# Performance work log

Hardware: AMD Instinct MI355X
Metric: run time of the kernel (lower is better)

Reference implementation:

```python
import jax, jax.numpy as jnp
import numpy as np


def _fwd_diffs(x, D, scale):
    # forward difference along each of the first D axes, zero at the end, scaled by x.shape[0]
    outs = []
    for d in range(D):
        pad = [(0, 0)] * x.ndim
        pad[d] = (0, 1)
        outs.append(jnp.pad(jnp.diff(x, axis=d), pad) * scale)
    return jnp.stack(outs, 0)


def _bwd_diffs(p, scale):
    # p: [D, *dims, l]; backward difference of p[i] along axis i with the torch narrow/cat semantics
    outs = []
    for i in range(p.shape[0]):
        pi = p[i]
        head = jax.lax.slice_in_dim(pi, 0, pi.shape[i] - 1, axis=i)
        z = jnp.zeros_like(jax.lax.slice_in_dim(pi, 0, 1, axis=i))
        before = jnp.concatenate([head, z], axis=i)
        after = jnp.concatenate([z, head], axis=i)
        outs.append((before - after) * scale)
    return jnp.stack(outs, 0)


def _solver(f, repeats, l, lmbda, nu):
    dims = list(f.shape)
    H = dims[0]
    D = len(dims) - 1
    res = 1.0 / H
    tauu = res / 6.0
    sigmap = res / (3.0 + l)
    sigmas = 1.0
    proj = l * (l - 1) // 2 + l
    tau = 1.0 / (2.0 + proj / 4.0)
    # (k1,k2) interval combinations and the membership matrix M[K,z] = (k1<=z<=k2)
    combos = np.array([(a, b) for a in range(l) for b in range(a, l)], dtype=np.int32)
    k1 = jnp.asarray(combos[:, 0])
    k2 = jnp.asarray(combos[:, 1])
    zz = np.arange(l)
    M = jnp.asarray(((combos[:, :1] <= zz) & (zz <= combos[:, 1:2])).astype(np.float32))  # [proj, l]

    img = jnp.broadcast_to(f[..., None], tuple(dims) + (l,))
    klf = jnp.arange(1, l + 1, dtype=f.dtype) / l - img  # k/l - f
    u = img
    ubar = img
    px = jnp.zeros((D,) + tuple(dims) + (l,), f.dtype)
    pt = jnp.zeros(tuple(dims) + (l,), f.dtype)
    sx = jnp.zeros((D,) + tuple(dims) + (proj,), f.dtype)
    mux = sx
    mubarx = sx
    nrj = jnp.zeros((), f.dtype)
    h_un = u

    for it in range(int(repeats)):
        # ---- parabola: dual ascent on (px,pt) with closed-form cubic (Cardano) projection ----
        musum = jnp.einsum('...p,pz->...z', mux, M)
        ux = px + sigmap * (_fwd_diffs(ubar, D, H) + musum)
        ut = pt + sigmap * (jnp.pad(jnp.diff(ubar, axis=-1), [(0, 0)] * (ubar.ndim - 1) + [(0, 1)]) * l)
        pen = lmbda * klf * klf
        B = 0.25 * jnp.sum(ux * ux, axis=0) - pen
        mask = ut < B
        y = ut + pen
        norm = jnp.sqrt(jnp.sum(ux * ux, axis=0))
        a = 0.5 * norm                                   # 2*0.25*norm
        b = (2.0 / 3.0) * (1.0 - 0.5 * y)
        sb = jnp.sqrt(jnp.maximum(-b, 0.0))              # sqrt(-b), only used where b<0
        d = jnp.where(b < 0, (a - sb ** 3) * (a + sb ** 3), a * a + b ** 3)
        c = jnp.power(a + jnp.sqrt(jnp.maximum(d, 0.0)), 1.0 / 3.0)
        mask1 = (d >= 0) & (c == 0)
        mask3 = d < 0
        sb3 = jnp.where(sb > 0, sb ** 3, 1.0)
        ratio = jnp.clip(a / sb3, -1.0, 1.0)
        c_safe = jnp.where(c == 0, 1.0, c)
        v = jnp.where(mask1, 0.0,
                      jnp.where(mask3, 2.0 * sb * jnp.cos(jnp.arccos(ratio) / 3.0), c - b / c_safe))
        norm_safe = jnp.where(norm == 0, 1.0, norm)
        px = jnp.where(mask[None],
                       jnp.where((norm == 0)[None], 0.0, (2.0 * v / norm_safe)[None] * ux),
                       ux)
        pt = jnp.where(mask, 0.25 * jnp.sum(px * px, axis=0) - pen, ut)

        # ---- l2 projection of s ----
        mx = sx - sigmas * mubarx
        snorm = jnp.sqrt(jnp.sum(mx * mx, axis=0))
        snorm_safe = jnp.where(snorm == 0, 1.0, snorm)
        sx = jnp.where((snorm > nu * H)[None], mx * nu / snorm_safe[None], mx)

        # ---- mu update: per-(k1,k2) partial sums over the label axis via cumsum ----
        cs = jnp.cumsum(px, axis=-1)
        cs = jnp.pad(cs, [(0, 0)] * (px.ndim - 1) + [(1, 0)])
        t = cs[..., k2 + 1] - cs[..., k1]                # [D, *dims, proj]
        mux_new = mux + tau * (sx - t)
        mubarx = 2.0 * mux_new - mux
        mux = mux_new

        # ---- clipping: primal update with box projection and boundary conditions ----
        if it % 10 == 0:
            h_un = u
        dx = _bwd_diffs(px, H)
        head = pt[..., :-1]
        z = jnp.zeros_like(pt[..., :1])
        dt = (jnp.concatenate([head, z], axis=-1) - jnp.concatenate([z, head], axis=-1)) * l
        Dv = u + tauu * (jnp.sum(dx, axis=0) + dt)
        un = jnp.clip(Dv, 0.0, 1.0)
        un = un.at[..., 0].set(1.0).at[..., l - 1].set(0.0)
        ubar = 2.0 * un - u
        u = un
        if it % 10 == 0:
            nrj = jnp.sum(jnp.abs(u - h_un))
    return u, nrj


def setup_inputs() -> dict:
    key = jax.random.key(0)
    H, W = 256, 256
    f = jax.random.uniform(key, (H, W, 1), dtype=jnp.float32)
    return {"f": f, "repeats": 10, "l": 16, "lmbda": 0.5, "nu": 0.1, "tol": 0.0}


def reference(f, repeats, l, lmbda, nu, tol):
    # tol/early-exit: tol=0 so the torch break never fires; iteration count is fixed at `repeats`.
    u, nrj = _solver(f, repeats, l, lmbda, nu)
    denom = float(np.prod(f.shape[:-1])) * l
    return (u, nrj, nrj / denom, 0)
```

## Files before the change

### kernel.cpp

```cpp
#include <hip/hip_runtime.h>

#define HH 256
#define WW 256
#define NPIX (HH*WW)
#define LL 16
#define NL (NPIX*LL)
#define PP 136
#define PP2 (PP*2)

typedef _Float16 half_t;
typedef __attribute__((ext_vector_type(8))) _Float16 half8;

static constexpr float SIGMAP_F = (float)((1.0/256.0)/(3.0+16.0));
static constexpr float TAUU_F   = (float)((1.0/256.0)/6.0);
static constexpr float TAU_F    = (float)(1.0/36.0);

__device__ __forceinline__ float clampf(float x, float lo, float hi){
    return fminf(fmaxf(x, lo), hi);
}
__device__ __forceinline__ half8 h8zero() {
    half8 v;
    #pragma unroll
    for (int i = 0; i < 8; ++i) v[i] = (half_t)0.0f;
    return v;
}

template<int MODE>
__global__ __launch_bounds__(256) void k_prox(const float* __restrict__ f,
    const half_t* __restrict__ ubar,
    const half_t* __restrict__ pxOld,
    half_t* __restrict__ pxCur,
    half_t* __restrict__ pt,
    const half_t* __restrict__ musum,
    float* __restrict__ nrj)
{
    int t = blockIdx.x*256 + threadIdx.x;
    if (MODE == 0 && t == 0) *nrj = 0.0f;
    int n  = t >> 1;
    int hf = t & 1;
    int z0 = hf << 3;
    int i = n >> 8, j = n & (WW-1);
    bool iok = (i < HH-1), jok = (j < WW-1);
    size_t base = (size_t)n*LL + z0;

    float fv = f[n];
    float g0c = 0.0f, g1c = 0.0f;
    half8 ubv = h8zero(), ubi = h8zero(), ubj = h8zero();
    float ubz8 = 0.0f;
    half8 ms0v = h8zero(), ms1v = h8zero();
    half8 p0v  = h8zero(), p1v  = h8zero(), ptv = h8zero();
    if (MODE == 0) {
        g0c = iok ? (f[n + WW] - fv) * 256.0f : 0.0f;
        g1c = jok ? (f[n + 1]  - fv) * 256.0f : 0.0f;
    } else {
        ubv = *reinterpret_cast<const half8*>(ubar + base);
        if (iok) ubi = *reinterpret_cast<const half8*>(ubar + base + (size_t)WW*LL);
        if (jok) ubj = *reinterpret_cast<const half8*>(ubar + base + LL);
        if (hf == 0) ubz8 = (float)ubar[base + 8];
        ms0v = *reinterpret_cast<const half8*>(musum + base);
        ms1v = *reinterpret_cast<const half8*>(musum + NL + base);
        p0v  = *reinterpret_cast<const half8*>(pxOld + base);
        p1v  = *reinterpret_cast<const half8*>(pxOld + NL + base);
        ptv  = *reinterpret_cast<const half8*>(pt + base);
    }

    half8 o0, o1, opt;
    #pragma unroll
    for (int e = 0; e < 8; ++e) {
        int z = z0 + e;
        float ux0, ux1, ut;
        if (MODE == 0) {
            ux0 = SIGMAP_F * g0c;
            ux1 = SIGMAP_F * g1c;
            ut  = 0.0f;
        } else {
            float ub = (float)ubv[e];
            float g0 = iok ? ((float)ubi[e] - ub) * 256.0f : 0.0f;
            float g1 = jok ? ((float)ubj[e] - ub) * 256.0f : 0.0f;
            float ubn = (e < 7) ? (float)ubv[e+1] : ubz8;
            float gt = (z < LL-1) ? (ubn - ub) * 16.0f : 0.0f;
            ux0 = (float)p0v[e] + SIGMAP_F * (g0 + (float)ms0v[e]);
            ux1 = (float)p1v[e] + SIGMAP_F * (g1 + (float)ms1v[e]);
            ut  = (float)ptv[e] + SIGMAP_F * gt;
        }

        float klf = (float)(z + 1) * 0.0625f - fv;
        float pen = 0.5f * klf * klf;

        float n2 = ux0*ux0 + ux1*ux1;
        float B  = 0.25f * n2 - pen;
        bool mask = ut < B;

        float px0 = ux0, px1 = ux1, ptn = ut;
        if (mask) {
            float y    = ut + pen;
            float norm = sqrtf(n2);
            float a    = 0.5f * norm;
            float b    = (2.0f/3.0f) * (1.0f - 0.5f*y);
            float v;
            if (b < 0.0f) {
                float sb  = sqrtf(-b);
                float sb3 = sb*sb*sb;
                float dd  = (a - sb3)*(a + sb3);
                if (dd < 0.0f) {
                    float ratio = clampf(a / sb3, -1.0f, 1.0f);
                    v = 2.0f * sb * cosf(acosf(ratio) * (1.0f/3.0f));
                } else {
                    float c = cbrtf(a + sqrtf(dd));
                    v = (c == 0.0f) ? 0.0f : (c - b/c);
                }
            } else {
                float dd = a*a + b*b*b;
                float c  = cbrtf(a + sqrtf(dd));
                v = (c == 0.0f) ? 0.0f : (c - b/c);
            }
            if (norm == 0.0f) { px0 = 0.0f; px1 = 0.0f; }
            else              { float s = 2.0f*v/norm; px0 = s*ux0; px1 = s*ux1; }
            ptn = 0.25f*(px0*px0 + px1*px1) - pen;
        }
        o0[e]  = (half_t)px0;
        o1[e]  = (half_t)px1;
        opt[e] = (half_t)ptn;
    }
    *reinterpret_cast<half8*>(pxCur + base)      = o0;
    *reinterpret_cast<half8*>(pxCur + NL + base) = o1;
    *reinterpret_cast<half8*>(pt + base)         = opt;
}

#define PH(k)  ((k) < 8 ? (float)ph0[(k)] : (float)ph1[(k)-8])
#define PPV(k) ((k) < 8 ? (float)pp0[(k)] : (float)pp1[(k)-8])

template<int H, int MODE>
__device__ __forceinline__ void do_set(int d, int n, int lane,
    half8 ph0, half8 ph1, half8 pp0, half8 pp1,
    const half_t* __restrict__ muC,
    half_t* __restrict__ muO,
    float* __restrict__ part)
{
    constexpr size_t setbase = (size_t)H * 17 * 2 * NPIX;
    const size_t vb   = setbase + (size_t)n*16 + (size_t)d*8;
    const size_t vb1  = vb + (size_t)16*NPIX;
    const size_t tail = setbase + (size_t)32*NPIX + (size_t)n*2 + (size_t)d;

    half8 mCv0 = h8zero(), mCv1 = h8zero(), mOv0 = h8zero(), mOv1 = h8zero();
    float mCT = 0.0f, mOT = 0.0f;
    if (MODE >= 1) {
        mCv0 = *reinterpret_cast<const half8*>(&muC[vb]);
        mCv1 = *reinterpret_cast<const half8*>(&muC[vb1]);
        mCT  = (float)muC[tail];
    }
    if (MODE == 2) {
        mOv0 = *reinterpret_cast<const half8*>(&muO[vb]);
        mOv1 = *reinterpret_cast<const half8*>(&muO[vb1]);
        mOT  = (float)muO[tail];
    }

    float tsA = 0.0f, tsB = 0.0f, tpA = 0.0f, tpB = 0.0f;
    #pragma unroll
    for (int k = H; k < 16; ++k) tsA += PH(k);
    #pragma unroll
    for (int k = 15-H; k < 16; ++k) tsB += PH(k);
    if (MODE >= 1) {
        #pragma unroll
        for (int k = H; k < 16; ++k) tpA += PPV(k);
        #pragma unroll
        for (int k = 15-H; k < 16; ++k) tpB += PPV(k);
    }

    half8 muo0, muo1;
    half_t muoT = (half_t)0.0f;
    float sA = 0.0f, sB = 0.0f;
    int q = 0;

    #pragma unroll
    for (int z = 15; z >= 0; --z) {
        float m = 0.0f;
        if (z >= H) {
            float mn;
            if (MODE == 0) {
                mn = -TAU_F * tsA;
            } else {
                float mC, mO;
                if (q < 8)       { mC=(float)mCv0[q];   mO=(float)mOv0[q]; }
                else if (q < 16) { mC=(float)mCv1[q-8]; mO=(float)mOv1[q-8]; }
                else             { mC=mCT;              mO=mOT; }
                float sxp = (mC - mO) * 36.0f + tpA;
                float mx  = sxp - (2.0f*mC - mO);
                float mo  = __shfl_xor(mx, 1);
                float snorm = sqrtf(mx*mx + mo*mo);
                if (snorm > 25.6f) mx *= 0.1f / snorm;
                mn = mC + TAU_F*(mx - tsA);
            }
            if (q < 8)       muo0[q]   = (half_t)mn;
            else if (q < 16) muo1[q-8] = (half_t)mn;
            else             muoT      = (half_t)mn;
            sA += mn;
            m  += sA;
            ++q;
        }
        if (z >= 15-H) {
            float mn;
            if (MODE == 0) {
                mn = -TAU_F * tsB;
            } else {
                float mC, mO;
                if (q < 8)       { mC=(float)mCv0[q];   mO=(float)mOv0[q]; }
                else if (q < 16) { mC=(float)mCv1[q-8]; mO=(float)mOv1[q-8]; }
                else             { mC=mCT;              mO=mOT; }
                float sxp = (mC - mO) * 36.0f + tpB;
                float mx  = sxp - (2.0f*mC - mO);
                float mo  = __shfl_xor(mx, 1);
                float snorm = sqrtf(mx*mx + mo*mo);
                if (snorm > 25.6f) mx *= 0.1f / snorm;
                mn = mC + TAU_F*(mx - tsB);
            }
            if (q < 8)       muo0[q]   = (half_t)mn;
            else if (q < 16) muo1[q-8] = (half_t)mn;
            else             muoT      = (half_t)mn;
            sB += mn;
            m  += sB;
            ++q;
        }
        if (z >= H+1) {
            tsA -= PH(z);
            if (MODE >= 1) tpA -= PPV(z);
        }
        if (z >= 15-H+1) {
            tsB -= PH(z);
            if (MODE >= 1) tpB -= PPV(z);
        }
        part[H*1024 + z*64 + lane] = m;
    }

    *reinterpret_cast<half8*>(&muO[vb])  = muo0;
    *reinterpret_cast<half8*>(&muO[vb1]) = muo1;
    muO[tail] = muoT;
}

template<int MODE>
__global__ __launch_bounds__(512, 4) void k_smu_u(
    const float* __restrict__ f,
    const half_t* __restrict__ pxCur,
    const half_t* __restrict__ pxOld,
    const half_t* __restrict__ pt,
    const half_t* __restrict__ muC,
    half_t* __restrict__ muO,
    half_t* __restrict__ musum,
    float* __restrict__ u, half_t* __restrict__ ubar,
    float* __restrict__ out,
    float* __restrict__ nrj, int last)
{
    __shared__ float part[8192];
    __shared__ float wsum[8];

    int tid  = threadIdx.x;
    int wv   = tid >> 6;
    int lane = tid & 63;
    int pix  = lane >> 1;
    int d    = lane & 1;
    int n    = blockIdx.x*32 + pix;

    const half8* pv = reinterpret_cast<const half8*>(pxCur + (size_t)d*NL + (size_t)n*LL);
    half8 ph0 = pv[0], ph1 = pv[1];
    half8 pp0 = h8zero(), pp1 = h8zero();
    if (MODE >= 1) {
        const half8* ppv = reinterpret_cast<const half8*>(pxOld + (size_t)d*NL + (size_t)n*LL);
        pp0 = ppv[0]; pp1 = ppv[1];
    }

    if      (wv == 0) do_set<0,MODE>(d,n,lane,ph0,ph1,pp0,pp1,muC,muO,part);
    else if (wv == 1) do_set<1,MODE>(d,n,lane,ph0,ph1,pp0,pp1,muC,muO,part);
    else if (wv == 2) do_set<2,MODE>(d,n,lane,ph0,ph1,pp0,pp1,muC,muO,part);
    else if (wv == 3) do_set<3,MODE>(d,n,lane,ph0,ph1,pp0,pp1,muC,muO,part);
    else if (wv == 4) do_set<4,MODE>(d,n,lane,ph0,ph1,pp0,pp1,muC,muO,part);
    else if (wv == 5) do_set<5,MODE>(d,n,lane,ph0,ph1,pp0,pp1,muC,muO,part);
    else if (wv == 6) do_set<6,MODE>(d,n,lane,ph0,ph1,pp0,pp1,muC,muO,part);
    else              do_set<7,MODE>(d,n,lane,ph0,ph1,pp0,pp1,muC,muO,part);

    __syncthreads();

    int t  = blockIdx.x*512 + tid;
    int z  = t & (LL-1);
    int n2 = t >> 4;
    int i2 = n2 >> 8;
    int j2 = n2 & (WW-1);
    float p0c = (float)pxCur[t];
    float p1c = (float)pxCur[NL + t];
    float p0u = (i2 > 0) ? (float)pxCur[t - WW*LL] : 0.0f;
    float p1l = (j2 > 0) ? (float)pxCur[NL + t - LL] : 0.0f;
    float ptc = (float)pt[t];
    float ptm = (z > 0) ? (float)pt[t - 1] : 0.0f;
    float uo  = (MODE == 0) ? f[n2] : u[t];

    #pragma unroll
    for (int r = 0; r < 2; ++r) {
        int z2    = (tid >> 6) + r*8;
        int inner = tid & 63;
        float s = 0.0f;
        #pragma unroll
        for (int hh = 0; hh < 8; ++hh) s += part[hh*1024 + z2*64 + inner];
        int d2 = inner & 1, pix2 = inner >> 1;
        musum[(size_t)d2*NL + ((size_t)blockIdx.x*32 + pix2)*LL + z2] = (half_t)s;
    }

    {
        float d0 = ((i2 < HH-1) ? p0c : 0.0f) - p0u;
        float d1 = ((j2 < WW-1) ? p1c : 0.0f) - p1l;
        float dt = ((z < LL-1) ? ptc : 0.0f) - ptm;

        float Dv = uo + TAUU_F * ((d0 + d1) * 256.0f + dt * 16.0f);
        float un = clampf(Dv, 0.0f, 1.0f);
        if (z == 0)     un = 1.0f;
        if (z == LL-1)  un = 0.0f;
        if (last) out[t] = un;
        else {
            u[t]    = un;
            ubar[t] = (half_t)(2.0f*un - uo);
        }

        if (MODE == 0) {
            float v = fabsf(un - uo);
            #pragma unroll
            for (int off = 32; off > 0; off >>= 1) v += __shfl_down(v, off);
            if ((tid & 63) == 0) wsum[wv] = v;
            __syncthreads();
            if (tid == 0) {
                float s = 0.0f;
                #pragma unroll
                for (int q = 0; q < 8; ++q) s += wsum[q];
                atomicAdd(nrj, s);
            }
        }
    }
}

__global__ void k_final(const float* __restrict__ nrj, float* __restrict__ out_tail)
{
    if (threadIdx.x == 0) {
        float e = *nrj;
        out_tail[0] = e;
        out_tail[1] = e * (1.0f/1048576.0f);
        out_tail[2] = 0.0f;
    }
}

extern "C" void kernel_launch(void* const* d_in, const int* in_sizes, int n_in,
                              void* d_out, int out_size, void* d_ws, size_t ws_size,
                              hipStream_t stream)
{
    const float* f = (const float*)d_in[0];
    float* out = (float*)d_out;

    char* w = (char*)d_ws;
    size_t off = 0;
    auto allocf = [&](size_t nfloats) {
        float* p = (float*)(w + off);
        off += nfloats * sizeof(float);
        return p;
    };
    auto alloch = [&](size_t nhalf) {
        half_t* p = (half_t*)(w + off);
        off += nhalf * sizeof(half_t);
        return p;
    };
    half_t* muA    = alloch((size_t)NPIX * PP2);
    half_t* muB    = alloch((size_t)NPIX * PP2);
    half_t* musum  = alloch(2*(size_t)NL);
    half_t* pxA    = alloch(2*(size_t)NL);
    half_t* pxB    = alloch(2*(size_t)NL);
    half_t* pt     = alloch((size_t)NL);
    half_t* ubar   = alloch((size_t)NL);
    float*  u      = allocf((size_t)NL);
    float*  nrj    = allocf(64);
    (void)ws_size; (void)in_sizes; (void)n_in; (void)out_size;

    half_t* pxC = pxA;
    half_t* pxO = pxB;
    half_t* mC  = muA;
    half_t* mO  = muB;
    for (int it = 0; it < 10; ++it) {
        int last = (it == 9) ? 1 : 0;
        if (it == 0) {
            k_prox<0><<<2*NPIX/256, 256, 0, stream>>>(f, ubar, pxO, pxC, pt, musum, nrj);
            k_smu_u<0><<<NPIX/32, 512, 0, stream>>>(f, pxC, pxO, pt, mC, mO, musum, u, ubar, out, nrj, last);
        } else if (it == 1) {
            k_prox<1><<<2*NPIX/256, 256, 0, stream>>>(f, ubar, pxO, pxC, pt, musum, nrj);
            k_smu_u<1><<<NPIX/32, 512, 0, stream>>>(f, pxC, pxO, pt, mC, mO, musum, u, ubar, out, nrj, last);
        } else {
            k_prox<1><<<2*NPIX/256, 256, 0, stream>>>(f, ubar, pxO, pxC, pt, musum, nrj);
            k_smu_u<2><<<NPIX/32, 512, 0, stream>>>(f, pxC, pxO, pt, mC, mO, musum, u, ubar, out, nrj, last);
        }
        { half_t* tmp = pxC; pxC = pxO; pxO = tmp; }
        { half_t* tmp = mC;  mC  = mO;  mO  = tmp; }
    }

    k_final<<<1, 64, 0, stream>>>(nrj, out + NL);
}
```

Measured before the change: 419.8 us.

## Fuse prox step into per-iteration kernel with halo recompute in LDS

Merges the separate prox kernel into the mu/u update kernel. Each block recomputes prox for its 32 pixels plus a halo (the row above and the left neighbour) and stages the results in shared memory. This removes one launch per iteration and the global round-trip of px/pt, at the cost of some redundant Cardano work and extra double-buffered state arrays. On the last iteration the kernel skips the mu/musum work entirely, and the energy atomic is replaced by per-block partials reduced in the final kernel.

```diff
diff --git a/kernel.cpp b/kernel.cpp
--- a/kernel.cpp
+++ b/kernel.cpp
@@ -7,6 +7,7 @@
 #define NL (NPIX*LL)
 #define PP 136
 #define PP2 (PP*2)
+#define NBLK (NPIX/32)
 
 typedef _Float16 half_t;
 typedef __attribute__((ext_vector_type(8))) _Float16 half8;
@@ -25,51 +26,43 @@
     return v;
 }
 
-template<int MODE>
-__global__ __launch_bounds__(256) void k_prox(const float* __restrict__ f,
-    const half_t* __restrict__ ubar,
-    const half_t* __restrict__ pxOld,
-    half_t* __restrict__ pxCur,
-    half_t* __restrict__ pt,
-    const half_t* __restrict__ musum,
-    float* __restrict__ nrj)
+template<int PM>
+__device__ __forceinline__ void prox_one(const float* __restrict__ f, int np, int hf,
+    const half_t* __restrict__ ubOld, const half_t* __restrict__ pxOld,
+    const half_t* __restrict__ ptOld, const half_t* __restrict__ msOld,
+    half8& o0, half8& o1, half8& opt)
 {
-    int t = blockIdx.x*256 + threadIdx.x;
-    if (MODE == 0 && t == 0) *nrj = 0.0f;
-    int n  = t >> 1;
-    int hf = t & 1;
     int z0 = hf << 3;
-    int i = n >> 8, j = n & (WW-1);
-    bool iok = (i < HH-1), jok = (j < WW-1);
-    size_t base = (size_t)n*LL + z0;
-
-    float fv = f[n];
+    int ip = np >> 8, jp = np & (WW-1);
+    bool iok = (ip < HH-1), jok = (jp < WW-1);
+    size_t base = (size_t)np*LL + z0;
+    float fv = f[np];
+
     float g0c = 0.0f, g1c = 0.0f;
     half8 ubv = h8zero(), ubi = h8zero(), ubj = h8zero();
     float ubz8 = 0.0f;
     half8 ms0v = h8zero(), ms1v = h8zero();
     half8 p0v  = h8zero(), p1v  = h8zero(), ptv = h8zero();
-    if (MODE == 0) {
-        g0c = iok ? (f[n + WW] - fv) * 256.0f : 0.0f;
-        g1c = jok ? (f[n + 1]  - fv) * 256.0f : 0.0f;
+    if (PM == 0) {
+        g0c = iok ? (f[np + WW] - fv) * 256.0f : 0.0f;
+        g1c = jok ? (f[np + 1]  - fv) * 256.0f : 0.0f;
     } else {
-        ubv = *reinterpret_cast<const half8*>(ubar + base);
-        if (iok) ubi = *reinterpret_cast<const half8*>(ubar + base + (size_t)WW*LL);
-        if (jok) ubj = *reinterpret_cast<const half8*>(ubar + base + LL);
-        if (hf == 0) ubz8 = (float)ubar[base + 8];
-        ms0v = *reinterpret_cast<const half8*>(musum + base);
-        ms1v = *reinterpret_cast<const half8*>(musum + NL + base);
+        ubv = *reinterpret_cast<const half8*>(ubOld + base);
+        if (iok) ubi = *reinterpret_cast<const half8*>(ubOld + base + (size_t)WW*LL);
+        if (jok) ubj = *reinterpret_cast<const half8*>(ubOld + base + LL);
+        if (hf == 0) ubz8 = (float)ubOld[base + 8];
+        ms0v = *reinterpret_cast<const half8*>(msOld + base);
+        ms1v = *reinterpret_cast<const half8*>(msOld + NL + base);
         p0v  = *reinterpret_cast<const half8*>(pxOld + base);
         p1v  = *reinterpret_cast<const half8*>(pxOld + NL + base);
-        ptv  = *reinterpret_cast<const half8*>(pt + base);
-    }
-
-    half8 o0, o1, opt;
+        ptv  = *reinterpret_cast<const half8*>(ptOld + base);
+    }
+
     #pragma unroll
     for (int e = 0; e < 8; ++e) {
         int z = z0 + e;
         float ux0, ux1, ut;
-        if (MODE == 0) {
+        if (PM == 0) {
             ux0 = SIGMAP_F * g0c;
             ux1 = SIGMAP_F * g1c;
             ut  = 0.0f;
@@ -122,9 +115,6 @@
         o1[e]  = (half_t)px1;
         opt[e] = (half_t)ptn;
     }
-    *reinterpret_cast<half8*>(pxCur + base)      = o0;
-    *reinterpret_cast<half8*>(pxCur + NL + base) = o1;
-    *reinterpret_cast<half8*>(pt + base)         = opt;
 }
 
 #define PH(k)  ((k) < 8 ? (float)ph0[(k)] : (float)ph1[(k)-8])
@@ -194,9 +184,7 @@
             if (q < 8)       muo0[q]   = (half_t)mn;
             else if (q < 16) muo1[q-8] = (half_t)mn;
             else             muoT      = (half_t)mn;
-            sA += mn;
-            m  += sA;
-            ++q;
+            sA += mn; m += sA; ++q;
         }
         if (z >= 15-H) {
             float mn;
@@ -217,9 +205,7 @@
             if (q < 8)       muo0[q]   = (half_t)mn;
             else if (q < 16) muo1[q-8] = (half_t)mn;
             else             muoT      = (half_t)mn;
-            sB += mn;
-            m  += sB;
-            ++q;
+            sB += mn; m += sB; ++q;
         }
         if (z >= H+1) {
             tsA -= PH(z);
@@ -238,72 +224,106 @@
 }
 
 template<int MODE>
-__global__ __launch_bounds__(512, 4) void k_smu_u(
+__global__ __launch_bounds__(512, 4) void k_iter(
     const float* __restrict__ f,
-    const half_t* __restrict__ pxCur,
-    const half_t* __restrict__ pxOld,
-    const half_t* __restrict__ pt,
-    const half_t* __restrict__ muC,
-    half_t* __restrict__ muO,
-    half_t* __restrict__ musum,
-    float* __restrict__ u, half_t* __restrict__ ubar,
-    float* __restrict__ out,
-    float* __restrict__ nrj, int last)
+    const half_t* __restrict__ pxOld, half_t* __restrict__ pxCur,
+    const half_t* __restrict__ ptOld, half_t* __restrict__ ptCur,
+    const half_t* __restrict__ ubOld, half_t* __restrict__ ubCur,
+    const half_t* __restrict__ msOld, half_t* __restrict__ msCur,
+    const half_t* __restrict__ muC, half_t* __restrict__ muO,
+    float* __restrict__ u, float* __restrict__ out,
+    float* __restrict__ nrjPartial)
 {
-    __shared__ float part[8192];
+    __shared__ float part[(MODE <= 2) ? 8192 : 1];
+    __shared__ __align__(16) half_t lp0[64][24];
+    __shared__ __align__(16) half_t lp1[33][24];
+    __shared__ __align__(16) half_t lpt[32][24];
     __shared__ float wsum[8];
 
-    int tid  = threadIdx.x;
-    int wv   = tid >> 6;
-    int lane = tid & 63;
-    int pix  = lane >> 1;
-    int d    = lane & 1;
-    int n    = blockIdx.x*32 + pix;
-
-    const half8* pv = reinterpret_cast<const half8*>(pxCur + (size_t)d*NL + (size_t)n*LL);
-    half8 ph0 = pv[0], ph1 = pv[1];
+    int tid = threadIdx.x;
+    int b   = blockIdx.x;
+    int n0  = b << 5;
+    int i0  = n0 >> 8;
+    int j0  = n0 & (WW-1);
+
+    if (tid < 130) {
+        int pl, np; bool valid = true;
+        int hf = tid & 1;
+        if (tid < 64)       { pl = tid >> 1;           np = n0 + pl; }
+        else if (tid < 128) { pl = 32 + ((tid-64)>>1); np = n0 + (pl-32) - WW; valid = (i0 > 0); }
+        else                { pl = 64;                 np = n0 - 1;            valid = (j0 > 0); }
+        if (valid) {
+            half8 o0, o1, opt;
+            prox_one<(MODE==0) ? 0 : 1>(f, np, hf, ubOld, pxOld, ptOld, msOld, o0, o1, opt);
+            int z0v = hf << 3;
+            if (pl < 64) *reinterpret_cast<half8*>(&lp0[pl][z0v]) = o0;
+            if (pl < 32) {
+                *reinterpret_cast<half8*>(&lp1[pl][z0v]) = o1;
+                *reinterpret_cast<half8*>(&lpt[pl][z0v]) = opt;
+                if (MODE <= 2) {
+                    *reinterpret_cast<half8*>(pxCur + (size_t)np*LL + z0v)      = o0;
+                    *reinterpret_cast<half8*>(pxCur + NL + (size_t)np*LL + z0v) = o1;
+                    *reinterpret_cast<half8*>(ptCur + (size_t)np*LL + z0v)      = opt;
+                }
+            } else if (pl == 64) {
+                *reinterpret_cast<half8*>(&lp1[32][z0v]) = o1;
+            }
+        }
+    }
+
+    int wv = tid >> 6, lane = tid & 63, pix = lane >> 1, d = lane & 1;
+    int n  = n0 + pix;
     half8 pp0 = h8zero(), pp1 = h8zero();
-    if (MODE >= 1) {
+    if (MODE == 1 || MODE == 2) {
         const half8* ppv = reinterpret_cast<const half8*>(pxOld + (size_t)d*NL + (size_t)n*LL);
         pp0 = ppv[0]; pp1 = ppv[1];
     }
-
-    if      (wv == 0) do_set<0,MODE>(d,n,lane,ph0,ph1,pp0,pp1,muC,muO,part);
-    else if (wv == 1) do_set<1,MODE>(d,n,lane,ph0,ph1,pp0,pp1,muC,muO,part);
-    else if (wv == 2) do_set<2,MODE>(d,n,lane,ph0,ph1,pp0,pp1,muC,muO,part);
-    else if (wv == 3) do_set<3,MODE>(d,n,lane,ph0,ph1,pp0,pp1,muC,muO,part);
-    else if (wv == 4) do_set<4,MODE>(d,n,lane,ph0,ph1,pp0,pp1,muC,muO,part);
-    else if (wv == 5) do_set<5,MODE>(d,n,lane,ph0,ph1,pp0,pp1,muC,muO,part);
-    else if (wv == 6) do_set<6,MODE>(d,n,lane,ph0,ph1,pp0,pp1,muC,muO,part);
-    else              do_set<7,MODE>(d,n,lane,ph0,ph1,pp0,pp1,muC,muO,part);
-
-    __syncthreads();
-
-    int t  = blockIdx.x*512 + tid;
+    int t  = b*512 + tid;
     int z  = t & (LL-1);
     int n2 = t >> 4;
     int i2 = n2 >> 8;
     int j2 = n2 & (WW-1);
-    float p0c = (float)pxCur[t];
-    float p1c = (float)pxCur[NL + t];
-    float p0u = (i2 > 0) ? (float)pxCur[t - WW*LL] : 0.0f;
-    float p1l = (j2 > 0) ? (float)pxCur[NL + t - LL] : 0.0f;
-    float ptc = (float)pt[t];
-    float ptm = (z > 0) ? (float)pt[t - 1] : 0.0f;
-    float uo  = (MODE == 0) ? f[n2] : u[t];
-
-    #pragma unroll
-    for (int r = 0; r < 2; ++r) {
-        int z2    = (tid >> 6) + r*8;
-        int inner = tid & 63;
-        float s = 0.0f;
+    float uo = (MODE == 0) ? f[n2] : u[t];
+
+    __syncthreads();
+
+    if (MODE <= 2) {
+        const half8* ls = (d == 0) ? reinterpret_cast<const half8*>(&lp0[pix][0])
+                                   : reinterpret_cast<const half8*>(&lp1[pix][0]);
+        half8 ph0 = ls[0], ph1 = ls[1];
+
+        if      (wv == 0) do_set<0,MODE>(d,n,lane,ph0,ph1,pp0,pp1,muC,muO,part);
+        else if (wv == 1) do_set<1,MODE>(d,n,lane,ph0,ph1,pp0,pp1,muC,muO,part);
+        else if (wv == 2) do_set<2,MODE>(d,n,lane,ph0,ph1,pp0,pp1,muC,muO,part);
+        else if (wv == 3) do_set<3,MODE>(d,n,lane,ph0,ph1,pp0,pp1,muC,muO,part);
+        else if (wv == 4) do_set<4,MODE>(d,n,lane,ph0,ph1,pp0,pp1,muC,muO,part);
+        else if (wv == 5) do_set<5,MODE>(d,n,lane,ph0,ph1,pp0,pp1,muC,muO,part);
+        else if (wv == 6) do_set<6,MODE>(d,n,lane,ph0,ph1,pp0,pp1,muC,muO,part);
+        else              do_set<7,MODE>(d,n,lane,ph0,ph1,pp0,pp1,muC,muO,part);
+
+        __syncthreads();
+
         #pragma unroll
-        for (int hh = 0; hh < 8; ++hh) s += part[hh*1024 + z2*64 + inner];
-        int d2 = inner & 1, pix2 = inner >> 1;
-        musum[(size_t)d2*NL + ((size_t)blockIdx.x*32 + pix2)*LL + z2] = (half_t)s;
+        for (int r = 0; r < 2; ++r) {
+            int z2    = (tid >> 6) + r*8;
+            int inner = tid & 63;
+            float s = 0.0f;
+            #pragma unroll
+            for (int hh = 0; hh < 8; ++hh) s += part[hh*1024 + z2*64 + inner];
+            int d2 = inner & 1, pix2 = inner >> 1;
+            msCur[(size_t)d2*NL + ((size_t)n0 + pix2)*LL + z2] = (half_t)s;
+        }
     }
 
     {
+        int pl2 = tid >> 4;
+        float p0c = (float)lp0[pl2][z];
+        float p1c = (float)lp1[pl2][z];
+        float p0u = (i2 > 0) ? (float)lp0[32 + pl2][z] : 0.0f;
+        float p1l = (j2 > 0) ? ((pl2 > 0) ? (float)lp1[pl2-1][z] : (float)lp1[32][z]) : 0.0f;
+        float ptc = (float)lpt[pl2][z];
+        float ptm = (z > 0) ? (float)lpt[pl2][z-1] : 0.0f;
+
         float d0 = ((i2 < HH-1) ? p0c : 0.0f) - p0u;
         float d1 = ((j2 < WW-1) ? p1c : 0.0f) - p1l;
         float dt = ((z < LL-1) ? ptc : 0.0f) - ptm;
@@ -312,10 +332,10 @@
         float un = clampf(Dv, 0.0f, 1.0f);
         if (z == 0)     un = 1.0f;
         if (z == LL-1)  un = 0.0f;
-        if (last) out[t] = un;
+        if (MODE == 3) out[t] = un;
         else {
-            u[t]    = un;
-            ubar[t] = (half_t)(2.0f*un - uo);
+            u[t]     = un;
+            ubCur[t] = (half_t)(2.0f*un - uo);
         }
 
         if (MODE == 0) {
@@ -327,19 +347,22 @@
             if (tid == 0) {
                 float s = 0.0f;
                 #pragma unroll
-                for (int q = 0; q < 8; ++q) s += wsum[q];
-                atomicAdd(nrj, s);
+                for (int q2 = 0; q2 < 8; ++q2) s += wsum[q2];
+                nrjPartial[b] = s;
             }
         }
     }
 }
 
-__global__ void k_final(const float* __restrict__ nrj, float* __restrict__ out_tail)
+__global__ void k_final(const float* __restrict__ nrjPartial, float* __restrict__ out_tail)
 {
+    float s = 0.0f;
+    for (int k = threadIdx.x; k < NBLK; k += 64) s += nrjPartial[k];
+    #pragma unroll
+    for (int off = 32; off > 0; off >>= 1) s += __shfl_down(s, off);
     if (threadIdx.x == 0) {
-        float e = *nrj;
-        out_tail[0] = e;
-        out_tail[1] = e * (1.0f/1048576.0f);
+        out_tail[0] = s;
+        out_tail[1] = s * (1.0f/1048576.0f);
         out_tail[2] = 0.0f;
     }
 }
@@ -363,36 +386,44 @@
         off += nhalf * sizeof(half_t);
         return p;
     };
-    half_t* muA    = alloch((size_t)NPIX * PP2);
-    half_t* muB    = alloch((size_t)NPIX * PP2);
-    half_t* musum  = alloch(2*(size_t)NL);
-    half_t* pxA    = alloch(2*(size_t)NL);
-    half_t* pxB    = alloch(2*(size_t)NL);
-    half_t* pt     = alloch((size_t)NL);
-    half_t* ubar   = alloch((size_t)NL);
-    float*  u      = allocf((size_t)NL);
-    float*  nrj    = allocf(64);
+    half_t* muA  = alloch((size_t)NPIX * PP2);
+    half_t* muB  = alloch((size_t)NPIX * PP2);
+    half_t* msA  = alloch(2*(size_t)NL);
+    half_t* msB  = alloch(2*(size_t)NL);
+    half_t* pxA  = alloch(2*(size_t)NL);
+    half_t* pxB  = alloch(2*(size_t)NL);
+    half_t* ptA  = alloch((size_t)NL);
+    half_t* ptB  = alloch((size_t)NL);
+    half_t* ubA  = alloch((size_t)NL);
+    half_t* ubB  = alloch((size_t)NL);
+    float*  u    = allocf((size_t)NL);
+    float*  nrjP = allocf(NBLK);
     (void)ws_size; (void)in_sizes; (void)n_in; (void)out_size;
 
-    half_t* pxC = pxA;
-    half_t* pxO = pxB;
-    half_t* mC  = muA;
-    half_t* mO  = muB;
+    half_t *pxO = pxA, *pxC = pxB;
+    half_t *ptO = ptA, *ptC = ptB;
+    half_t *ubO = ubA, *ubC = ubB;
+    half_t *msO = msA, *msC = msB;
+    half_t *mC  = muA, *mO  = muB;
     for (int it = 0; it < 10; ++it) {
-        int last = (it == 9) ? 1 : 0;
-        if (it == 0) {
-            k_prox<0><<<2*NPIX/256, 256, 0, stream>>>(f, ubar, pxO, pxC, pt, musum, nrj);
-            k_smu_u<0><<<NPIX/32, 512, 0, stream>>>(f, pxC, pxO, pt, mC, mO, musum, u, ubar, out, nrj, last);
-        } else if (it == 1) {
-            k_prox<1><<<2*NPIX/256, 256, 0, stream>>>(f, ubar, pxO, pxC, pt, musum, nrj);
-            k_smu_u<1><<<NPIX/32, 512, 0, stream>>>(f, pxC, pxO, pt, mC, mO, musum, u, ubar, out, nrj, last);
-        } else {
-            k_prox<1><<<2*NPIX/256, 256, 0, stream>>>(f, ubar, pxO, pxC, pt, musum, nrj);
-            k_smu_u<2><<<NPIX/32, 512, 0, stream>>>(f, pxC, pxO, pt, mC, mO, musum, u, ubar, out, nrj, last);
-        }
-        { half_t* tmp = pxC; pxC = pxO; pxO = tmp; }
+        if (it == 0)
+            k_iter<0><<<NBLK, 512, 0, stream>>>(f, pxO, pxC, ptO, ptC, ubO, ubC,
+                                                msO, msC, mC, mO, u, out, nrjP);
+        else if (it == 1)
+            k_iter<1><<<NBLK, 512, 0, stream>>>(f, pxO, pxC, ptO, ptC, ubO, ubC,
+                                                msO, msC, mC, mO, u, out, nrjP);
+        else if (it < 9)
+            k_iter<2><<<NBLK, 512, 0, stream>>>(f, pxO, pxC, ptO, ptC, ubO, ubC,
+                                                msO, msC, mC, mO, u, out, nrjP);
+        else
+            k_iter<3><<<NBLK, 512, 0, stream>>>(f, pxO, pxC, ptO, ptC, ubO, ubC,
+                                                msO, msC, mC, mO, u, out, nrjP);
+        { half_t* tmp = pxO; pxO = pxC; pxC = tmp; }
+        { half_t* tmp = ptO; ptO = ptC; ptC = tmp; }
+        { half_t* tmp = ubO; ubO = ubC; ubC = tmp; }
+        { half_t* tmp = msO; msO = msC; msC = tmp; }
         { half_t* tmp = mC;  mC  = mO;  mO  = tmp; }
     }
 
-    k_final<<<1, 64, 0, stream>>>(nrj, out + NL);
-}
+    k_final<<<1, 64, 0, stream>>>(nrjP, out + NL);
+}
```

New measurement: 406.9 us. 3.1% less time.
